# Kernel tuning notes

Hardware: AMD Instinct MI355X
Metric: run time of the kernel (lower is better)

## Reference

```python
import jax, jax.numpy as jnp
import numpy as np

K = 20
BN_EPS = 1e-5


def setup_inputs() -> dict:
    key = jax.random.key(0)
    ks = jax.random.split(key, 8)
    B, N, C = 4, 8192, 128
    x = jax.random.normal(ks[0], (B, C, N), dtype=jnp.float32)
    xyz = jax.random.normal(ks[1], (B, N, 3), dtype=jnp.float32)
    # Conv1d(C+3 -> C, kernel_size=1): weight [C, C+3], bias [C]
    w1 = jax.random.normal(ks[2], (C, C + 3), dtype=jnp.float32) * 0.05
    b1 = jax.random.normal(ks[3], (C,), dtype=jnp.float32) * 0.05
    gamma = jnp.ones((C,), dtype=jnp.float32)
    beta = jnp.zeros((C,), dtype=jnp.float32)
    # Conv1d(C -> C, kernel_size=1)
    w2 = jax.random.normal(ks[4], (C, C), dtype=jnp.float32) * 0.05
    b2 = jax.random.normal(ks[5], (C,), dtype=jnp.float32) * 0.05
    return {"x": x, "xyz": xyz, "w1": w1, "b1": b1, "gamma": gamma,
            "beta": beta, "w2": w2, "b2": b2}


def _compute_normals(xyz):
    # xyz: [B, N, 3]
    sq = jnp.sum(xyz * xyz, axis=-1)                      # [B, N]
    dist = (-2.0 * jnp.einsum('bnc,bmc->bnm', xyz, xyz)
            + sq[:, :, None] + sq[:, None, :])            # [B, N, N]
    _, idx = jax.lax.top_k(-dist, K)                      # smallest-k -> [B, N, k]
    neighbors = jax.vmap(lambda pts, ix: pts[ix])(xyz, idx)  # [B, N, k, 3]
    nb = neighbors - xyz[:, :, None, :]                   # centered
    cov = jnp.einsum('bnkc,bnkd->bncd', nb, nb)           # [B, N, 3, 3]
    _, eigvecs = jnp.linalg.eigh(cov)                     # ascending eigenvalues
    return eigvecs[..., :, 0]                             # normal = smallest-eig vector, [B, N, 3]


def reference(x, xyz, w1, b1, gamma, beta, w2, b2):
    normals = _compute_normals(xyz)                       # [B, N, 3]
    geo = jnp.concatenate([x, jnp.transpose(normals, (0, 2, 1))], axis=1)  # [B, C+3, N]
    h = jnp.einsum('oc,bcn->bon', w1, geo) + b1[None, :, None]
    # BatchNorm1d (training mode, biased variance over (B, N))
    mean = jnp.mean(h, axis=(0, 2), keepdims=True)
    var = jnp.mean((h - mean) ** 2, axis=(0, 2), keepdims=True)
    h = gamma[None, :, None] * (h - mean) * jax.lax.rsqrt(var + BN_EPS) + beta[None, :, None]
    h = jax.nn.relu(h)
    out = jnp.einsum('oc,bcn->bon', w2, h) + b2[None, :, None]
    return out
```

## Files before the change

kernel.cpp:

```cpp
#include <hip/hip_runtime.h>
#include <math.h>

#define N_PTS 8192
#define BATCH 4
#define CH 128
#define KNN 20
#define CAP 91
#define STQ 93
#define POOL 256


__device__ __forceinline__ float slapy2f(float x, float y) {
#pragma clang fp contract(off)
  float ax = fabsf(x), ay = fabsf(y);
  float w = fmaxf(ax, ay), z = fminf(ax, ay);
  if (z == 0.0f) return w;
  float t = z / w;
  return w * sqrtf(1.0f + t * t);
}

__device__ __forceinline__ void slartgf(float f, float g, float* cs, float* sn, float* r) {
#pragma clang fp contract(off)
  if (g == 0.0f) { *cs = 1.0f; *sn = 0.0f; *r = f; }
  else if (f == 0.0f) { *cs = 0.0f; *sn = copysignf(1.0f, g); *r = fabsf(g); }
  else {
    float f1 = fabsf(f);
    float d = sqrtf(f * f + g * g);
    *cs = f1 / d;
    *r = copysignf(d, f);
    *sn = g / (*r);
  }
}

__device__ void slaev2f(float a, float b, float c, float* rt1, float* rt2,
                        float* cs1, float* sn1) {
#pragma clang fp contract(off)
  float sm = a + c, df = a - c, adf = fabsf(df);
  float tb = b + b, ab = fabsf(tb);
  float acmx, acmn;
  if (fabsf(a) > fabsf(c)) { acmx = a; acmn = c; } else { acmx = c; acmn = a; }
  float rt;
  if (adf > ab)      { float q = ab / adf;  rt = adf * sqrtf(1.0f + q * q); }
  else if (adf < ab) { float q = adf / ab;  rt = ab * sqrtf(1.0f + q * q); }
  else               rt = ab * sqrtf(2.0f);
  int sgn1;
  if (sm < 0.0f)      { *rt1 = 0.5f * (sm - rt); sgn1 = -1; *rt2 = (acmx / *rt1) * acmn - (b / *rt1) * b; }
  else if (sm > 0.0f) { *rt1 = 0.5f * (sm + rt); sgn1 = 1;  *rt2 = (acmx / *rt1) * acmn - (b / *rt1) * b; }
  else                { *rt1 = 0.5f * rt; *rt2 = -0.5f * rt; sgn1 = 1; }
  float cs; int sgn2;
  if (df >= 0.0f) { cs = df + rt; sgn2 = 1; } else { cs = df - rt; sgn2 = -1; }
  float acs = fabsf(cs);
  if (acs > ab) {
    float ct = -tb / cs;
    *sn1 = 1.0f / sqrtf(1.0f + ct * ct);
    *cs1 = ct * (*sn1);
  } else {
    if (ab == 0.0f) { *cs1 = 1.0f; *sn1 = 0.0f; }
    else {
      float tn = -cs / tb;
      *cs1 = 1.0f / sqrtf(1.0f + tn * tn);
      *sn1 = tn * (*cs1);
    }
  }
  if (sgn1 == sgn2) { float tn = *cs1; *cs1 = -(*sn1); *sn1 = tn; }
}

__device__ void eigh3_smallest(float a00, float a10, float a20,
                               float a11, float a21, float a22, float evec[3]) {
#pragma clang fp contract(off)
  float d[3], e[2], tau = 0.0f, v2 = 0.0f;
  d[0] = a00;
  {
    float xnorm = sqrtf(a20 * a20);
    if (xnorm == 0.0f) {
      tau = 0.0f; v2 = 0.0f;
      e[0] = a10; d[1] = a11; e[1] = a21; d[2] = a22;
    } else {
      float alpha = a10;
      float beta = -copysignf(slapy2f(alpha, xnorm), alpha);
      tau = (beta - alpha) / beta;
      float invs = 1.0f / (alpha - beta);
      v2 = a20 * invs;
      e[0] = beta;
      float y0 = tau * a11;
      float y1 = tau * a21;
      y0 = y0 + tau * (a21 * v2);
      y1 = y1 + (tau * v2) * a22;
      float dot = y0 + y1 * v2;
      float al = (-0.5f * tau) * dot;
      float w0 = y0 + al;
      float w1 = y1 + al * v2;
      a11 = (a11 - w0) - w0;
      a21 = (a21 - v2 * w0) - w1;
      a22 = (a22 - v2 * w1) - w1 * v2;
      d[1] = a11; e[1] = a21; d[2] = a22;
    }
  }

  float z[3][3] = {{1.0f,0.0f,0.0f},{0.0f,1.0f,0.0f},{0.0f,0.0f,1.0f}};
  const float eps = 5.9604644775390625e-08f;
  const float eps2 = 3.5527136788005009e-15f;
  const float safmin = 1.1754943508222875e-38f;
  int nmaxit = 90, jtot = 0;
  int l1 = 0;
  int l, m, lend, lsv, lendsv;
  float p, g, r, c, s, f, b_, rt1, rt2, tst;
  float wc[2], wsn[2];

outer_loop:
  if (l1 > 2) goto sorting;
  if (l1 > 0) e[l1 - 1] = 0.0f;
  {
    int mm;
    for (mm = l1; mm <= 1; ++mm) {
      tst = fabsf(e[mm]);
      if (tst == 0.0f) break;
      if (tst <= (sqrtf(fabsf(d[mm])) * sqrtf(fabsf(d[mm + 1]))) * eps) { e[mm] = 0.0f; break; }
    }
    m = (mm > 1) ? 2 : mm;
  }
  l = l1; lsv = l; lend = m; lendsv = lend; l1 = m + 1;
  if (lend == l) goto outer_loop;
  {
    float an = 0.0f;
    for (int i2 = l; i2 <= lend; ++i2) an = fmaxf(an, fabsf(d[i2]));
    for (int i2 = l; i2 < lend; ++i2) an = fmaxf(an, fabsf(e[i2]));
    if (an == 0.0f) goto outer_loop;
  }
  if (fabsf(d[lend]) < fabsf(d[l])) { lend = lsv; l = lendsv; }

  if (lend > l) {
ql40:
    if (l != lend) {
      for (m = l; m <= lend - 1; ++m) {
        tst = e[m] * e[m];
        if (tst <= (eps2 * fabsf(d[m])) * fabsf(d[m + 1]) + safmin) goto ql60;
      }
    }
    m = lend;
ql60:
    if (m < lend) e[m] = 0.0f;
    p = d[l];
    if (m == l) goto ql80;
    if (m == l + 1) {
      slaev2f(d[l], e[l], d[l + 1], &rt1, &rt2, &c, &s);
      for (int i2 = 0; i2 < 3; ++i2) {
        float temp = z[i2][l + 1];
        z[i2][l + 1] = c * temp - s * z[i2][l];
        z[i2][l]     = s * temp + c * z[i2][l];
      }
      d[l] = rt1; d[l + 1] = rt2; e[l] = 0.0f;
      l += 2;
      if (l <= lend) goto ql40;
      goto done140;
    }
    if (jtot == nmaxit) goto done140;
    jtot++;
    g = (d[l + 1] - p) / (2.0f * e[l]);
    r = slapy2f(g, 1.0f);
    g = d[m] - p + e[l] / (g + copysignf(r, g));
    s = 1.0f; c = 1.0f; p = 0.0f;
    for (int i2 = m - 1; i2 >= l; --i2) {
      f = s * e[i2]; b_ = c * e[i2];
      slartgf(g, f, &c, &s, &r);
      if (i2 != m - 1) e[i2 + 1] = r;
      g = d[i2 + 1] - p;
      r = (d[i2] - g) * s + 2.0f * c * b_;
      p = s * r;
      d[i2 + 1] = g + p;
      g = c * r - b_;
      wc[i2] = c; wsn[i2] = -s;
    }
    for (int j = m - 1; j >= l; --j) {
      float ct = wc[j], st = wsn[j];
      for (int i2 = 0; i2 < 3; ++i2) {
        float temp = z[i2][j + 1];
        z[i2][j + 1] = ct * temp - st * z[i2][j];
        z[i2][j]     = st * temp + ct * z[i2][j];
      }
    }
    d[l] -= p;
    e[l] = g;
    goto ql40;
ql80:
    d[l] = p;
    l += 1;
    if (l <= lend) goto ql40;
    goto done140;
  } else {
qr90:
    if (l != lend) {
      for (m = l; m >= lend + 1; --m) {
        tst = e[m - 1] * e[m - 1];
        if (tst <= (eps2 * fabsf(d[m])) * fabsf(d[m - 1]) + safmin) goto qr110;
      }
    }
    m = lend;
qr110:
    if (m > lend) e[m - 1] = 0.0f;
    p = d[l];
    if (m == l) goto qr130;
    if (m == l - 1) {
      slaev2f(d[l - 1], e[l - 1], d[l], &rt1, &rt2, &c, &s);
      for (int i2 = 0; i2 < 3; ++i2) {
        float temp = z[i2][l];
        z[i2][l]     = c * temp - s * z[i2][l - 1];
        z[i2][l - 1] = s * temp + c * z[i2][l - 1];
      }
      d[l - 1] = rt1; d[l] = rt2; e[l - 1] = 0.0f;
      l -= 2;
      if (l >= lend) goto qr90;
      goto done140;
    }
    if (jtot == nmaxit) goto done140;
    jtot++;
    g = (d[l - 1] - p) / (2.0f * e[l - 1]);
    r = slapy2f(g, 1.0f);
    g = d[m] - p + e[l - 1] / (g + copysignf(r, g));
    s = 1.0f; c = 1.0f; p = 0.0f;
    for (int i2 = m; i2 <= l - 1; ++i2) {
      f = s * e[i2]; b_ = c * e[i2];
      slartgf(g, f, &c, &s, &r);
      if (i2 != m) e[i2 - 1] = r;
      g = d[i2] - p;
      r = (d[i2 + 1] - g) * s + 2.0f * c * b_;
      p = s * r;
      d[i2] = g + p;
      g = c * r - b_;
      wc[i2] = c; wsn[i2] = s;
    }
    for (int j = m; j <= l - 1; ++j) {
      float ct = wc[j], st = wsn[j];
      for (int i2 = 0; i2 < 3; ++i2) {
        float temp = z[i2][j + 1];
        z[i2][j + 1] = ct * temp - st * z[i2][j];
        z[i2][j]     = st * temp + ct * z[i2][j];
      }
    }
    d[l] -= p;
    e[l - 1] = g;
    goto qr90;
qr130:
    d[l] = p;
    l -= 1;
    if (l >= lend) goto qr90;
    goto done140;
  }
done140:
  if (jtot < nmaxit) goto outer_loop;
sorting:
  for (int ii = 1; ii <= 2; ++ii) {
    int i_ = ii - 1, k = i_;
    p = d[i_];
    for (int j = ii; j <= 2; ++j) if (d[j] < p) { k = j; p = d[j]; }
    if (k != i_) {
      d[k] = d[i_]; d[i_] = p;
      for (int i2 = 0; i2 < 3; ++i2) { float tz = z[i2][i_]; z[i2][i_] = z[i2][k]; z[i2][k] = tz; }
    }
  }
  {
    float z10 = z[1][0], z20 = z[2][0];
    float sum = z10 + v2 * z20;
    evec[0] = z[0][0];
    evec[1] = z10 - tau * sum;
    evec[2] = z20 - tau * sum * v2;
  }
}

__global__ __launch_bounds__(256) void prep_kernel(const float* __restrict__ xyz,
                                                   const float* __restrict__ w1,
                                                   const float* __restrict__ w2,
                                                   float4* __restrict__ xyz4,
                                                   float* __restrict__ w1t,
                                                   float* __restrict__ w2t,
                                                   float* __restrict__ stats) {
  int idx = blockIdx.x * 256 + threadIdx.x;
  if (idx < BATCH * N_PTS) {
    float x = xyz[idx * 3], y = xyz[idx * 3 + 1], zz = xyz[idx * 3 + 2];
    float sq = fmaf(zz, zz, fmaf(y, y, x * x));
    xyz4[idx] = make_float4(x, y, zz, -0.5f * sq);
  }
  if (idx < 132 * CH) {
    int cc = idx >> 7, o = idx & 127;
    w1t[idx] = (cc < 131) ? w1[o * 131 + cc] : 0.0f;
  }
  if (idx < CH * CH) {
    int cc = idx >> 7, o = idx & 127;
    w2t[idx] = w2[o * CH + cc];
  }
  if (idx < 256) stats[idx] = 0.0f;
}

__device__ __forceinline__ float qdist2(const float4 qv, const float4 cv) {
  float dot = fmaf(qv.x, cv.x, fmaf(qv.y, cv.y, qv.z * cv.z));
  return fmaf(-2.0f, dot, (-2.0f * qv.w) + (-2.0f * cv.w));
}

__device__ __forceinline__ unsigned int distbits(float dist) {
  unsigned int du = __float_as_uint(dist);
  return (du & 0x80000000u) ? ~du : (du | 0x80000000u);
}

__global__ __launch_bounds__(512, 8) void knn_select_kernel(const float4* __restrict__ xyz4,
                                                            unsigned short* __restrict__ nidx) {
  __shared__ unsigned long long pool[POOL];
  __shared__ unsigned int lst_d[64 * STQ];
  __shared__ unsigned short lst_i[64 * STQ];
  __shared__ float bnd[8 * 64];
  __shared__ unsigned int qcnt[64];
  __shared__ unsigned int qflag[64];
  __shared__ unsigned int qover[64];
  __shared__ unsigned int pool_cnt;

  const int t = threadIdx.x;
  const int w = t >> 6, l = t & 63;
  const int batch = blockIdx.x >> 7;
  const int q0 = (blockIdx.x & 127) << 6;
  const float4* __restrict__ xb = xyz4 + batch * N_PTS;
  const float4 qv = xb[q0 + l];
  const float qw = -2.0f * qv.w;

  if (t < 64) { qcnt[t] = 0; qflag[t] = 0; qover[t] = 0; }
  if (t == 0) pool_cnt = 0;
  __syncthreads();

  const int base = __builtin_amdgcn_readfirstlane(w * 1024);

  float c0 = -INFINITY, c1 = -INFINITY, c2 = -INFINITY;
#pragma unroll 8
  for (int i = 0; i < 1024; ++i) {
    float4 cv = xb[base + i];
    float k = fmaf(qv.x, cv.x, fmaf(qv.y, cv.y, fmaf(qv.z, cv.z, cv.w)));
    float t0 = fminf(c0, k); c0 = fmaxf(c0, k);
    float t1 = fminf(c1, t0); c1 = fmaxf(c1, t0);
    c2 = fmaxf(c2, t1);
  }
  bnd[w * 64 + l] = c2;
  __syncthreads();

  float kmin = bnd[l];
#pragma unroll
  for (int ww = 1; ww < 8; ++ww) kmin = fminf(kmin, bnd[ww * 64 + l]);
  float Tq = fmaf(-2.0f, kmin, qw);
  Tq = Tq + (fabsf(Tq) * 2e-5f + 1e-3f);
  const float thK = 0.5f * (qw - Tq) - 1e-3f;

#pragma unroll 4
  for (int i = 0; i < 1024; ++i) {
    float4 cv = xb[base + i];
    float k = fmaf(qv.x, cv.x, fmaf(qv.y, cv.y, fmaf(qv.z, cv.z, cv.w)));
    if (k >= thK) {
      float dot = fmaf(qv.x, cv.x, fmaf(qv.y, cv.y, qv.z * cv.z));
      float dist = fmaf(-2.0f, dot, qw + (-2.0f * cv.w));
      if (dist <= Tq) {
        unsigned int db = distbits(dist);
        unsigned int pos = atomicAdd(&qcnt[l], 1u);
        if (pos < CAP) {
          lst_d[l * STQ + pos] = db;
          lst_i[l * STQ + pos] = (unsigned short)(base + i);
        } else {
          unsigned long long key = ((unsigned long long)db << 32)
                                 | ((unsigned int)l << 16) | (unsigned int)(base + i);
          unsigned int pp = atomicAdd(&pool_cnt, 1u);
          if (pp < POOL) { pool[pp] = key; qflag[l] = 1u; }
          else qover[l] = 1u;
        }
      }
    }
  }
  __syncthreads();

  const int qg = t >> 3, sub = t & 7;
  unsigned int n = qcnt[qg]; if (n > CAP) n = CAP;
  const unsigned int pcnt = (qflag[qg] && !qover[qg]) ? min(pool_cnt, (unsigned int)POOL) : 0u;
  unsigned short* oq = nidx + ((size_t)(batch * N_PTS + q0 + qg)) * KNN;

  if (qover[qg]) {
    if (sub == 0) {
      unsigned long long best[KNN];
#pragma unroll
      for (int j = 0; j < KNN; ++j) best[j] = ~0ULL;
      const float4 qv2 = xb[q0 + qg];
      for (int m = 0; m < N_PTS; ++m) {
        float dist = qdist2(qv2, xb[m]);
        unsigned long long p = ((unsigned long long)distbits(dist) << 32) | (unsigned int)m;
        if (p < best[KNN - 1]) {
          int j = KNN - 1;
          while (j > 0 && best[j - 1] > p) { best[j] = best[j - 1]; --j; }
          best[j] = p;
        }
      }
      for (int j = 0; j < KNN; ++j) oq[j] = (unsigned short)(best[j] & 0xffffu);
    }
  } else {
    for (int r = 0; r < KNN; ++r) {
      unsigned long long best = ~0ULL; int bslot = 0;
      for (unsigned int s = sub; s < n; s += 8) {
        unsigned long long v = ((unsigned long long)lst_d[qg * STQ + s] << 16)
                             | (unsigned long long)lst_i[qg * STQ + s];
        if (v < best) { best = v; bslot = (int)s; }
      }
      for (unsigned int s = sub; s < pcnt; s += 8) {
        unsigned long long v = pool[s];
        if ((unsigned int)((v >> 16) & 0xffffu) == (unsigned int)qg) {
          unsigned long long pv = ((v >> 32) << 16) | (v & 0xffffULL);
          if (pv < best) { best = pv; bslot = 0x10000 | (int)s; }
        }
      }
#pragma unroll
      for (int mm = 1; mm < 8; mm <<= 1) {
        unsigned long long ob = __shfl_xor(best, mm, 64);
        int obs = __shfl_xor(bslot, mm, 64);
        if (ob < best) { best = ob; bslot = obs; }
      }
      int s = bslot & 0xffff;
      if ((s & 7) == sub) {
        if (bslot & 0x10000) pool[s] = ~0ULL;
        else lst_d[qg * STQ + s] = 0xFFFFFFFFu;
      }
      if (sub == 0) oq[r] = (unsigned short)(best & 0xffffu);
    }
  }
}

__global__ __launch_bounds__(256) void normals_kernel(const float4* __restrict__ xyz4,
                                                      const unsigned short* __restrict__ nidx,
                                                      float4* __restrict__ nrm4) {
  int gid = blockIdx.x * 256 + threadIdx.x;
  int batch = gid >> 13, q = gid & (N_PTS - 1);
  const float4* __restrict__ xb = xyz4 + batch * N_PTS;
  const float4 qv = xb[q];
  const unsigned short* iq = nidx + (size_t)gid * KNN;
  float c00, c01, c02, c11, c12, c22;
  {
#pragma clang fp contract(off)
    c00 = 0.f; c01 = 0.f; c02 = 0.f; c11 = 0.f; c12 = 0.f; c22 = 0.f;
    for (int j = 0; j < KNN; ++j) {
      float4 pv = xb[iq[j]];
      float dx = pv.x - qv.x, dy = pv.y - qv.y, dz = pv.z - qv.z;
      c00 = c00 + dx * dx; c01 = c01 + dx * dy; c02 = c02 + dx * dz;
      c11 = c11 + dy * dy; c12 = c12 + dy * dz; c22 = c22 + dz * dz;
    }
  }
  float ev[3];
  eigh3_smallest(c00, c01, c02, c11, c12, c22, ev);
  nrm4[gid] = make_float4(ev[0], ev[1], ev[2], 0.0f);
}

__global__ __launch_bounds__(256) void gemm1_stats_kernel(const float* __restrict__ x,
                                                          const float4* __restrict__ nrm4,
                                                          const float* __restrict__ w1t,
                                                          const float* __restrict__ b1,
                                                          float* __restrict__ sums,
                                                          float* __restrict__ sumsq) {
  __shared__ float lds[64 * 134];
  const int t = threadIdx.x;
  const int b = blockIdx.x >> 7;
  const int n0 = (blockIdx.x & 127) << 6;
  for (int idx = t; idx < CH * 64; idx += 256) {
    int cc = idx >> 6, nl = idx & 63;
    lds[nl * 134 + cc] = x[((size_t)(b * CH + cc)) * N_PTS + n0 + nl];
  }
  if (t < 64) {
    float4 nv = nrm4[b * N_PTS + n0 + t];
    lds[t * 134 + 128] = nv.x; lds[t * 134 + 129] = nv.y;
    lds[t * 134 + 130] = nv.z; lds[t * 134 + 131] = 0.0f;
  }
  __syncthreads();

  const int og = __builtin_amdgcn_readfirstlane(t >> 6);
  const int nl = t & 63;
  float acc[32];
#pragma unroll
  for (int k = 0; k < 32; ++k) acc[k] = b1[og * 32 + k];
  for (int c2 = 0; c2 < 66; ++c2) {
    float2 xv = *(const float2*)&lds[nl * 134 + 2 * c2];
    const float* wr0 = w1t + (2 * c2) * CH + og * 32;
    const float* wr1 = wr0 + CH;
#pragma unroll
    for (int k = 0; k < 32; ++k) acc[k] = fmaf(wr0[k], xv.x, acc[k]);
#pragma unroll
    for (int k = 0; k < 32; ++k) acc[k] = fmaf(wr1[k], xv.y, acc[k]);
  }
  __syncthreads();
#pragma unroll
  for (int k2 = 0; k2 < 16; ++k2)
    *(float2*)&lds[nl * 134 + og * 32 + 2 * k2] = make_float2(acc[2 * k2], acc[2 * k2 + 1]);
  __syncthreads();
  {
    int cc = t & 127, hf = t >> 7;
    float sm = 0.f, sq = 0.f;
    for (int rr = hf * 32; rr < hf * 32 + 32; ++rr) {
      float v = lds[rr * 134 + cc];
      sm += v; sq = fmaf(v, v, sq);
    }
    atomicAdd(&sums[cc], sm);
    atomicAdd(&sumsq[cc], sq);
  }
}

__global__ void bn_finalize_kernel(const float* __restrict__ sums, const float* __restrict__ sumsq,
                                   const float* __restrict__ gamma, const float* __restrict__ beta,
                                   float* __restrict__ scale, float* __restrict__ shift) {
  int c = threadIdx.x;
  if (c < CH) {
    const double cnt = (double)(BATCH * N_PTS);
    double mean = (double)sums[c] / cnt;
    double var = (double)sumsq[c] / cnt - mean * mean;
    double inv = 1.0 / sqrt(var + 1e-5);
    double sc = (double)gamma[c] * inv;
    scale[c] = (float)sc;
    shift[c] = (float)((double)beta[c] - mean * sc);
  }
}

__global__ __launch_bounds__(256) void fused_out_kernel(const float* __restrict__ x,
                                                        const float4* __restrict__ nrm4,
                                                        const float* __restrict__ w1t,
                                                        const float* __restrict__ b1,
                                                        const float* __restrict__ w2t,
                                                        const float* __restrict__ b2,
                                                        const float* __restrict__ scale,
                                                        const float* __restrict__ shift,
                                                        float* __restrict__ out) {
  __shared__ float lds[64 * 134];
  const int t = threadIdx.x;
  const int b = blockIdx.x >> 7;
  const int n0 = (blockIdx.x & 127) << 6;
  for (int idx = t; idx < CH * 64; idx += 256) {
    int cc = idx >> 6, nl = idx & 63;
    lds[nl * 134 + cc] = x[((size_t)(b * CH + cc)) * N_PTS + n0 + nl];
  }
  if (t < 64) {
    float4 nv = nrm4[b * N_PTS + n0 + t];
    lds[t * 134 + 128] = nv.x; lds[t * 134 + 129] = nv.y;
    lds[t * 134 + 130] = nv.z; lds[t * 134 + 131] = 0.0f;
  }
  __syncthreads();

  const int og = __builtin_amdgcn_readfirstlane(t >> 6);
  const int nl = t & 63;
  float acc[32];
#pragma unroll
  for (int k = 0; k < 32; ++k) acc[k] = b1[og * 32 + k];
  for (int c2 = 0; c2 < 66; ++c2) {
    float2 xv = *(const float2*)&lds[nl * 134 + 2 * c2];
    const float* wr0 = w1t + (2 * c2) * CH + og * 32;
    const float* wr1 = wr0 + CH;
#pragma unroll
    for (int k = 0; k < 32; ++k) acc[k] = fmaf(wr0[k], xv.x, acc[k]);
#pragma unroll
    for (int k = 0; k < 32; ++k) acc[k] = fmaf(wr1[k], xv.y, acc[k]);
  }
#pragma unroll
  for (int k = 0; k < 32; ++k) {
    float sc = scale[og * 32 + k], sh = shift[og * 32 + k];
    acc[k] = fmaxf(fmaf(acc[k], sc, sh), 0.0f);
  }
  __syncthreads();
#pragma unroll
  for (int k2 = 0; k2 < 16; ++k2)
    *(float2*)&lds[nl * 134 + og * 32 + 2 * k2] = make_float2(acc[2 * k2], acc[2 * k2 + 1]);
  __syncthreads();

  float acc2[32];
#pragma unroll
  for (int k = 0; k < 32; ++k) acc2[k] = b2[og * 32 + k];
  for (int c2 = 0; c2 < 64; ++c2) {
    float2 hv = *(const float2*)&lds[nl * 134 + 2 * c2];
    const float* wr0 = w2t + (2 * c2) * CH + og * 32;
    const float* wr1 = wr0 + CH;
#pragma unroll
    for (int k = 0; k < 32; ++k) acc2[k] = fmaf(wr0[k], hv.x, acc2[k]);
#pragma unroll
    for (int k = 0; k < 32; ++k) acc2[k] = fmaf(wr1[k], hv.y, acc2[k]);
  }
#pragma unroll
  for (int k = 0; k < 32; ++k) {
    int o = og * 32 + k;
    out[((size_t)(b * CH + o)) * N_PTS + n0 + nl] = acc2[k];
  }
}

extern "C" void kernel_launch(void* const* d_in, const int* in_sizes, int n_in,
                              void* d_out, int out_size, void* d_ws, size_t ws_size,
                              hipStream_t stream) {
  const float* x     = (const float*)d_in[0];
  const float* xyz   = (const float*)d_in[1];
  const float* w1    = (const float*)d_in[2];
  const float* b1    = (const float*)d_in[3];
  const float* gamma = (const float*)d_in[4];
  const float* beta  = (const float*)d_in[5];
  const float* w2    = (const float*)d_in[6];
  const float* b2    = (const float*)d_in[7];
  float* out = (float*)d_out;

  float* W = (float*)d_ws;
  float4* xyz4 = (float4*)W;
  float4* nrm4 = (float4*)(W + 131072);
  float* w1t   = W + 262144;
  float* w2t   = W + 279040;
  float* stats = W + 295424;
  float* scale = W + 295680;
  float* shift = W + 295808;
  unsigned short* nidx = (unsigned short*)(W + 295936);

  prep_kernel<<<128, 256, 0, stream>>>(xyz, w1, w2, xyz4, w1t, w2t, stats);
  knn_select_kernel<<<BATCH * N_PTS / 64, 512, 0, stream>>>(xyz4, nidx);
  normals_kernel<<<BATCH * N_PTS / 256, 256, 0, stream>>>(xyz4, nidx, nrm4);
  gemm1_stats_kernel<<<BATCH * N_PTS / 64, 256, 0, stream>>>(x, nrm4, w1t, b1, stats, stats + 128);
  bn_finalize_kernel<<<1, 128, 0, stream>>>(stats, stats + 128, gamma, beta, scale, shift);
  fused_out_kernel<<<BATCH * N_PTS / 64, 256, 0, stream>>>(x, nrm4, w1t, b1, w2t, b2, scale, shift, out);
}
```

Baseline: 396.3 us.

## Process two query groups per 1024-thread KNN block and shrink normals blocks

The KNN select kernel now handles 128 queries per block with 16 waves, each scanning 512 candidates. Each wave keeps a top-2 per query and merges wave pairs to get a third-smallest bound. Candidate loads are shared across the two query sets in the bound pass, and the bound buffer is aliased with the candidate lists in shared memory. The two query halves are filtered and selected one after the other, with 16 lanes per query in the selection step, and the list capacity is raised. The normals kernel switches to 64-thread blocks. This cuts repeated candidate reads and raises selection parallelism, at the cost of a looser threshold, more barriers and a larger block footprint.

```diff
diff --git a/kernel.cpp b/kernel.cpp
--- a/kernel.cpp
+++ b/kernel.cpp
@@ -5,9 +5,11 @@
 #define BATCH 4
 #define CH 128
 #define KNN 20
-#define CAP 91
-#define STQ 93
+#define CAP 112
+#define STQ 114
 #define POOL 256
+#define QPB 128
+#define NW 16
 
 
 __device__ __forceinline__ float slapy2f(float x, float y) {
@@ -301,58 +303,78 @@
   return (du & 0x80000000u) ? ~du : (du | 0x80000000u);
 }
 
-__global__ __launch_bounds__(512, 8) void knn_select_kernel(const float4* __restrict__ xyz4,
-                                                            unsigned short* __restrict__ nidx) {
+__global__ __launch_bounds__(1024) void knn_select_kernel(const float4* __restrict__ xyz4,
+                                                          unsigned short* __restrict__ nidx) {
+  __shared__ alignas(16) unsigned char smem[64 * STQ * 6];
   __shared__ unsigned long long pool[POOL];
-  __shared__ unsigned int lst_d[64 * STQ];
-  __shared__ unsigned short lst_i[64 * STQ];
-  __shared__ float bnd[8 * 64];
   __shared__ unsigned int qcnt[64];
   __shared__ unsigned int qflag[64];
   __shared__ unsigned int qover[64];
   __shared__ unsigned int pool_cnt;
 
+  float2* bnd2 = reinterpret_cast<float2*>(smem);
+  unsigned int* lst_d = reinterpret_cast<unsigned int*>(smem);
+  unsigned short* lst_i = reinterpret_cast<unsigned short*>(smem + 64 * STQ * 4);
+
   const int t = threadIdx.x;
   const int w = t >> 6, l = t & 63;
-  const int batch = blockIdx.x >> 7;
-  const int q0 = (blockIdx.x & 127) << 6;
+  const int batch = blockIdx.x >> 6;
+  const int q0 = (blockIdx.x & 63) << 7;
   const float4* __restrict__ xb = xyz4 + batch * N_PTS;
-  const float4 qv = xb[q0 + l];
-  const float qw = -2.0f * qv.w;
-
+  const float4 qvA = xb[q0 + l];
+  const float4 qvB = xb[q0 + 64 + l];
+  const float qwA = -2.0f * qvA.w;
+  const float qwB = -2.0f * qvB.w;
+
+  const int base = __builtin_amdgcn_readfirstlane(w << 9);
+
+  float a0 = -INFINITY, a1 = -INFINITY;
+  float c0 = -INFINITY, c1 = -INFINITY;
+#pragma unroll 8
+  for (int i = 0; i < 512; ++i) {
+    float4 cv = xb[base + i];
+    float kA = fmaf(qvA.x, cv.x, fmaf(qvA.y, cv.y, fmaf(qvA.z, cv.z, cv.w)));
+    float kB = fmaf(qvB.x, cv.x, fmaf(qvB.y, cv.y, fmaf(qvB.z, cv.z, cv.w)));
+    float tA = fminf(a0, kA); a0 = fmaxf(a0, kA); a1 = fmaxf(a1, tA);
+    float tB = fminf(c0, kB); c0 = fmaxf(c0, kB); c1 = fmaxf(c1, tB);
+  }
+  bnd2[w * 128 + l]      = make_float2(a0, a1);
+  bnd2[w * 128 + 64 + l] = make_float2(c0, c1);
+  __syncthreads();
+
+  float TqA, thKA, TqB, thKB;
+  {
+    float kminA = INFINITY, kminB = INFINITY;
+#pragma unroll
+    for (int g = 0; g < 8; ++g) {
+      float2 pa = bnd2[(2 * g) * 128 + l];
+      float2 pb = bnd2[(2 * g + 1) * 128 + l];
+      float v3 = fmaxf(fminf(pa.y, pb.x), fminf(pa.x, pb.y));
+      kminA = fminf(kminA, v3);
+      float2 qa = bnd2[(2 * g) * 128 + 64 + l];
+      float2 qb = bnd2[(2 * g + 1) * 128 + 64 + l];
+      float u3 = fmaxf(fminf(qa.y, qb.x), fminf(qa.x, qb.y));
+      kminB = fminf(kminB, u3);
+    }
+    TqA = fmaf(-2.0f, kminA, qwA);
+    TqA = TqA + (fabsf(TqA) * 2e-5f + 1e-3f);
+    thKA = 0.5f * (qwA - TqA) - 1e-3f;
+    TqB = fmaf(-2.0f, kminB, qwB);
+    TqB = TqB + (fabsf(TqB) * 2e-5f + 1e-3f);
+    thKB = 0.5f * (qwB - TqB) - 1e-3f;
+  }
   if (t < 64) { qcnt[t] = 0; qflag[t] = 0; qover[t] = 0; }
   if (t == 0) pool_cnt = 0;
   __syncthreads();
 
-  const int base = __builtin_amdgcn_readfirstlane(w * 1024);
-
-  float c0 = -INFINITY, c1 = -INFINITY, c2 = -INFINITY;
-#pragma unroll 8
-  for (int i = 0; i < 1024; ++i) {
+#pragma unroll 4
+  for (int i = 0; i < 512; ++i) {
     float4 cv = xb[base + i];
-    float k = fmaf(qv.x, cv.x, fmaf(qv.y, cv.y, fmaf(qv.z, cv.z, cv.w)));
-    float t0 = fminf(c0, k); c0 = fmaxf(c0, k);
-    float t1 = fminf(c1, t0); c1 = fmaxf(c1, t0);
-    c2 = fmaxf(c2, t1);
-  }
-  bnd[w * 64 + l] = c2;
-  __syncthreads();
-
-  float kmin = bnd[l];
-#pragma unroll
-  for (int ww = 1; ww < 8; ++ww) kmin = fminf(kmin, bnd[ww * 64 + l]);
-  float Tq = fmaf(-2.0f, kmin, qw);
-  Tq = Tq + (fabsf(Tq) * 2e-5f + 1e-3f);
-  const float thK = 0.5f * (qw - Tq) - 1e-3f;
-
-#pragma unroll 4
-  for (int i = 0; i < 1024; ++i) {
-    float4 cv = xb[base + i];
-    float k = fmaf(qv.x, cv.x, fmaf(qv.y, cv.y, fmaf(qv.z, cv.z, cv.w)));
-    if (k >= thK) {
-      float dot = fmaf(qv.x, cv.x, fmaf(qv.y, cv.y, qv.z * cv.z));
-      float dist = fmaf(-2.0f, dot, qw + (-2.0f * cv.w));
-      if (dist <= Tq) {
+    float k = fmaf(qvA.x, cv.x, fmaf(qvA.y, cv.y, fmaf(qvA.z, cv.z, cv.w)));
+    if (k >= thKA) {
+      float dot = fmaf(qvA.x, cv.x, fmaf(qvA.y, cv.y, qvA.z * cv.z));
+      float dist = fmaf(-2.0f, dot, qwA + (-2.0f * cv.w));
+      if (dist <= TqA) {
         unsigned int db = distbits(dist);
         unsigned int pos = atomicAdd(&qcnt[l], 1u);
         if (pos < CAP) {
@@ -370,63 +392,149 @@
   }
   __syncthreads();
 
-  const int qg = t >> 3, sub = t & 7;
-  unsigned int n = qcnt[qg]; if (n > CAP) n = CAP;
-  const unsigned int pcnt = (qflag[qg] && !qover[qg]) ? min(pool_cnt, (unsigned int)POOL) : 0u;
-  unsigned short* oq = nidx + ((size_t)(batch * N_PTS + q0 + qg)) * KNN;
-
-  if (qover[qg]) {
-    if (sub == 0) {
-      unsigned long long best[KNN];
-#pragma unroll
-      for (int j = 0; j < KNN; ++j) best[j] = ~0ULL;
-      const float4 qv2 = xb[q0 + qg];
-      for (int m = 0; m < N_PTS; ++m) {
-        float dist = qdist2(qv2, xb[m]);
-        unsigned long long p = ((unsigned long long)distbits(dist) << 32) | (unsigned int)m;
-        if (p < best[KNN - 1]) {
-          int j = KNN - 1;
-          while (j > 0 && best[j - 1] > p) { best[j] = best[j - 1]; --j; }
-          best[j] = p;
-        }
-      }
-      for (int j = 0; j < KNN; ++j) oq[j] = (unsigned short)(best[j] & 0xffffu);
-    }
-  } else {
-    for (int r = 0; r < KNN; ++r) {
-      unsigned long long best = ~0ULL; int bslot = 0;
-      for (unsigned int s = sub; s < n; s += 8) {
-        unsigned long long v = ((unsigned long long)lst_d[qg * STQ + s] << 16)
-                             | (unsigned long long)lst_i[qg * STQ + s];
-        if (v < best) { best = v; bslot = (int)s; }
-      }
-      for (unsigned int s = sub; s < pcnt; s += 8) {
-        unsigned long long v = pool[s];
-        if ((unsigned int)((v >> 16) & 0xffffu) == (unsigned int)qg) {
-          unsigned long long pv = ((v >> 32) << 16) | (v & 0xffffULL);
-          if (pv < best) { best = pv; bslot = 0x10000 | (int)s; }
-        }
-      }
-#pragma unroll
-      for (int mm = 1; mm < 8; mm <<= 1) {
-        unsigned long long ob = __shfl_xor(best, mm, 64);
-        int obs = __shfl_xor(bslot, mm, 64);
-        if (ob < best) { best = ob; bslot = obs; }
-      }
-      int s = bslot & 0xffff;
-      if ((s & 7) == sub) {
-        if (bslot & 0x10000) pool[s] = ~0ULL;
-        else lst_d[qg * STQ + s] = 0xFFFFFFFFu;
-      }
-      if (sub == 0) oq[r] = (unsigned short)(best & 0xffffu);
-    }
-  }
-}
-
-__global__ __launch_bounds__(256) void normals_kernel(const float4* __restrict__ xyz4,
-                                                      const unsigned short* __restrict__ nidx,
-                                                      float4* __restrict__ nrm4) {
-  int gid = blockIdx.x * 256 + threadIdx.x;
+  {
+    const int qg = t >> 4, sub = t & 15;
+    unsigned int n = qcnt[qg]; if (n > CAP) n = CAP;
+    const unsigned int pcnt = (qflag[qg] && !qover[qg]) ? min(pool_cnt, (unsigned int)POOL) : 0u;
+    unsigned short* oq = nidx + ((size_t)(batch * N_PTS + q0 + qg)) * KNN;
+
+    if (qover[qg]) {
+      if (sub == 0) {
+        unsigned long long best[KNN];
+#pragma unroll
+        for (int j = 0; j < KNN; ++j) best[j] = ~0ULL;
+        const float4 qv2 = xb[q0 + qg];
+        for (int m = 0; m < N_PTS; ++m) {
+          float dist = qdist2(qv2, xb[m]);
+          unsigned long long p = ((unsigned long long)distbits(dist) << 32) | (unsigned int)m;
+          if (p < best[KNN - 1]) {
+            int j = KNN - 1;
+            while (j > 0 && best[j - 1] > p) { best[j] = best[j - 1]; --j; }
+            best[j] = p;
+          }
+        }
+        for (int j = 0; j < KNN; ++j) oq[j] = (unsigned short)(best[j] & 0xffffu);
+      }
+    } else {
+      for (int r = 0; r < KNN; ++r) {
+        unsigned long long best = ~0ULL; int bslot = 0;
+        for (unsigned int s = sub; s < n; s += 16) {
+          unsigned long long v = ((unsigned long long)lst_d[qg * STQ + s] << 16)
+                               | (unsigned long long)lst_i[qg * STQ + s];
+          if (v < best) { best = v; bslot = (int)s; }
+        }
+        for (unsigned int s = sub; s < pcnt; s += 16) {
+          unsigned long long v = pool[s];
+          if ((unsigned int)((v >> 16) & 0xffffu) == (unsigned int)qg) {
+            unsigned long long pv = ((v >> 32) << 16) | (v & 0xffffULL);
+            if (pv < best) { best = pv; bslot = 0x10000 | (int)s; }
+          }
+        }
+#pragma unroll
+        for (int mm = 1; mm < 16; mm <<= 1) {
+          unsigned long long ob = __shfl_xor(best, mm, 64);
+          int obs = __shfl_xor(bslot, mm, 64);
+          if (ob < best) { best = ob; bslot = obs; }
+        }
+        int s = bslot & 0xffff;
+        if ((s & 15) == sub) {
+          if (bslot & 0x10000) pool[s] = ~0ULL;
+          else lst_d[qg * STQ + s] = 0xFFFFFFFFu;
+        }
+        if (sub == 0) oq[r] = (unsigned short)(best & 0xffffu);
+      }
+    }
+  }
+  __syncthreads();
+
+  if (t < 64) { qcnt[t] = 0; qflag[t] = 0; qover[t] = 0; }
+  if (t == 0) pool_cnt = 0;
+  __syncthreads();
+
+#pragma unroll 4
+  for (int i = 0; i < 512; ++i) {
+    float4 cv = xb[base + i];
+    float k = fmaf(qvB.x, cv.x, fmaf(qvB.y, cv.y, fmaf(qvB.z, cv.z, cv.w)));
+    if (k >= thKB) {
+      float dot = fmaf(qvB.x, cv.x, fmaf(qvB.y, cv.y, qvB.z * cv.z));
+      float dist = fmaf(-2.0f, dot, qwB + (-2.0f * cv.w));
+      if (dist <= TqB) {
+        unsigned int db = distbits(dist);
+        unsigned int pos = atomicAdd(&qcnt[l], 1u);
+        if (pos < CAP) {
+          lst_d[l * STQ + pos] = db;
+          lst_i[l * STQ + pos] = (unsigned short)(base + i);
+        } else {
+          unsigned long long key = ((unsigned long long)db << 32)
+                                 | ((unsigned int)l << 16) | (unsigned int)(base + i);
+          unsigned int pp = atomicAdd(&pool_cnt, 1u);
+          if (pp < POOL) { pool[pp] = key; qflag[l] = 1u; }
+          else qover[l] = 1u;
+        }
+      }
+    }
+  }
+  __syncthreads();
+
+  {
+    const int qg = t >> 4, sub = t & 15;
+    unsigned int n = qcnt[qg]; if (n > CAP) n = CAP;
+    const unsigned int pcnt = (qflag[qg] && !qover[qg]) ? min(pool_cnt, (unsigned int)POOL) : 0u;
+    unsigned short* oq = nidx + ((size_t)(batch * N_PTS + q0 + 64 + qg)) * KNN;
+
+    if (qover[qg]) {
+      if (sub == 0) {
+        unsigned long long best[KNN];
+#pragma unroll
+        for (int j = 0; j < KNN; ++j) best[j] = ~0ULL;
+        const float4 qv2 = xb[q0 + 64 + qg];
+        for (int m = 0; m < N_PTS; ++m) {
+          float dist = qdist2(qv2, xb[m]);
+          unsigned long long p = ((unsigned long long)distbits(dist) << 32) | (unsigned int)m;
+          if (p < best[KNN - 1]) {
+            int j = KNN - 1;
+            while (j > 0 && best[j - 1] > p) { best[j] = best[j - 1]; --j; }
+            best[j] = p;
+          }
+        }
+        for (int j = 0; j < KNN; ++j) oq[j] = (unsigned short)(best[j] & 0xffffu);
+      }
+    } else {
+      for (int r = 0; r < KNN; ++r) {
+        unsigned long long best = ~0ULL; int bslot = 0;
+        for (unsigned int s = sub; s < n; s += 16) {
+          unsigned long long v = ((unsigned long long)lst_d[qg * STQ + s] << 16)
+                               | (unsigned long long)lst_i[qg * STQ + s];
+          if (v < best) { best = v; bslot = (int)s; }
+        }
+        for (unsigned int s = sub; s < pcnt; s += 16) {
+          unsigned long long v = pool[s];
+          if ((unsigned int)((v >> 16) & 0xffffu) == (unsigned int)qg) {
+            unsigned long long pv = ((v >> 32) << 16) | (v & 0xffffULL);
+            if (pv < best) { best = pv; bslot = 0x10000 | (int)s; }
+          }
+        }
+#pragma unroll
+        for (int mm = 1; mm < 16; mm <<= 1) {
+          unsigned long long ob = __shfl_xor(best, mm, 64);
+          int obs = __shfl_xor(bslot, mm, 64);
+          if (ob < best) { best = ob; bslot = obs; }
+        }
+        int s = bslot & 0xffff;
+        if ((s & 15) == sub) {
+          if (bslot & 0x10000) pool[s] = ~0ULL;
+          else lst_d[qg * STQ + s] = 0xFFFFFFFFu;
+        }
+        if (sub == 0) oq[r] = (unsigned short)(best & 0xffffu);
+      }
+    }
+  }
+}
+
+__global__ __launch_bounds__(64) void normals_kernel(const float4* __restrict__ xyz4,
+                                                     const unsigned short* __restrict__ nidx,
+                                                     float4* __restrict__ nrm4) {
+  int gid = blockIdx.x * 64 + threadIdx.x;
   int batch = gid >> 13, q = gid & (N_PTS - 1);
   const float4* __restrict__ xb = xyz4 + batch * N_PTS;
   const float4 qv = xb[q];
@@ -606,8 +714,8 @@
   unsigned short* nidx = (unsigned short*)(W + 295936);
 
   prep_kernel<<<128, 256, 0, stream>>>(xyz, w1, w2, xyz4, w1t, w2t, stats);
-  knn_select_kernel<<<BATCH * N_PTS / 64, 512, 0, stream>>>(xyz4, nidx);
-  normals_kernel<<<BATCH * N_PTS / 256, 256, 0, stream>>>(xyz4, nidx, nrm4);
+  knn_select_kernel<<<BATCH * N_PTS / QPB, 1024, 0, stream>>>(xyz4, nidx);
+  normals_kernel<<<BATCH * N_PTS / 64, 64, 0, stream>>>(xyz4, nidx, nrm4);
   gemm1_stats_kernel<<<BATCH * N_PTS / 64, 256, 0, stream>>>(x, nrm4, w1t, b1, stats, stats + 128);
   bn_finalize_kernel<<<1, 128, 0, stream>>>(stats, stats + 128, gamma, beta, scale, shift);
   fused_out_kernel<<<BATCH * N_PTS / 64, 256, 0, stream>>>(x, nrm4, w1t, b1, w2t, b2, scale, shift, out);
```

New measurement: 418.6 us. +5.6%, slower.

## Split KNN candidate scan across 16 waves with pairwise top-3 threshold merge

Applied to the files above, without the earlier changes.

The KNN select kernel now launches 1024 threads, so each wave scans 512 candidates instead of 1024, with a small register prefetch buffer in both passes. Each wave keeps its top three keys, and adjacent waves' lists are merged to get a tighter per-query pruning bound. Per-query list capacity grows and the final top-20 extraction uses 16 lanes per query instead of 8. The normals kernel moves to 64-thread blocks. The larger shared-memory footprint and 1024-thread blocks may limit how many blocks fit per CU, and the prefetch reads a few entries past each batch's slice.

```diff
diff --git a/kernel.cpp b/kernel.cpp
--- a/kernel.cpp
+++ b/kernel.cpp
@@ -5,8 +5,8 @@
 #define BATCH 4
 #define CH 128
 #define KNN 20
-#define CAP 91
-#define STQ 93
+#define CAP 112
+#define STQ 114
 #define POOL 256
 
 
@@ -301,12 +301,12 @@
   return (du & 0x80000000u) ? ~du : (du | 0x80000000u);
 }
 
-__global__ __launch_bounds__(512, 8) void knn_select_kernel(const float4* __restrict__ xyz4,
-                                                            unsigned short* __restrict__ nidx) {
-  __shared__ unsigned long long pool[POOL];
+__global__ __launch_bounds__(1024, 8) void knn_select_kernel(const float4* __restrict__ xyz4,
+                                                             unsigned short* __restrict__ nidx) {
   __shared__ unsigned int lst_d[64 * STQ];
   __shared__ unsigned short lst_i[64 * STQ];
-  __shared__ float bnd[8 * 64];
+  __shared__ float bnd[16 * 64 * 3];
+  __shared__ unsigned long long pool[POOL];
   __shared__ unsigned int qcnt[64];
   __shared__ unsigned int qflag[64];
   __shared__ unsigned int qover[64];
@@ -322,55 +322,80 @@
 
   if (t < 64) { qcnt[t] = 0; qflag[t] = 0; qover[t] = 0; }
   if (t == 0) pool_cnt = 0;
-  __syncthreads();
-
-  const int base = __builtin_amdgcn_readfirstlane(w * 1024);
-
-  float c0 = -INFINITY, c1 = -INFINITY, c2 = -INFINITY;
-#pragma unroll 8
-  for (int i = 0; i < 1024; ++i) {
-    float4 cv = xb[base + i];
-    float k = fmaf(qv.x, cv.x, fmaf(qv.y, cv.y, fmaf(qv.z, cv.z, cv.w)));
-    float t0 = fminf(c0, k); c0 = fmaxf(c0, k);
-    float t1 = fminf(c1, t0); c1 = fmaxf(c1, t0);
-    c2 = fmaxf(c2, t1);
-  }
-  bnd[w * 64 + l] = c2;
-  __syncthreads();
-
-  float kmin = bnd[l];
-#pragma unroll
-  for (int ww = 1; ww < 8; ++ww) kmin = fminf(kmin, bnd[ww * 64 + l]);
+
+  const int base = __builtin_amdgcn_readfirstlane(w * 512);
+
+  float a0 = -INFINITY, a1 = -INFINITY, a2 = -INFINITY;
+  {
+    float4 buf[4];
+#pragma unroll
+    for (int j = 0; j < 4; ++j) buf[j] = xb[base + j];
+    for (int i = 0; i < 512; i += 4) {
+#pragma unroll
+      for (int j = 0; j < 4; ++j) {
+        float4 cv = buf[j];
+        buf[j] = xb[base + i + 4 + j];
+        float k = fmaf(qv.x, cv.x, fmaf(qv.y, cv.y, fmaf(qv.z, cv.z, cv.w)));
+        float t0 = fminf(a0, k); a0 = fmaxf(a0, k);
+        float t1 = fminf(a1, t0); a1 = fmaxf(a1, t0);
+        a2 = fmaxf(a2, t1);
+      }
+    }
+  }
+  {
+    int bi = (w * 64 + l) * 3;
+    bnd[bi] = a0; bnd[bi + 1] = a1; bnd[bi + 2] = a2;
+  }
+  __syncthreads();
+
+  float kmin = INFINITY;
+#pragma unroll
+  for (int g = 0; g < 8; ++g) {
+    int ai = ((2 * g) * 64 + l) * 3;
+    int bi = ((2 * g + 1) * 64 + l) * 3;
+    float pa0 = bnd[ai], pa1 = bnd[ai + 1], pa2 = bnd[ai + 2];
+    float pb0 = bnd[bi], pb1 = bnd[bi + 1], pb2 = bnd[bi + 2];
+    float third = fmaxf(fmaxf(pa2, pb2), fmaxf(fminf(pa1, pb0), fminf(pa0, pb1)));
+    kmin = fminf(kmin, third);
+  }
   float Tq = fmaf(-2.0f, kmin, qw);
   Tq = Tq + (fabsf(Tq) * 2e-5f + 1e-3f);
   const float thK = 0.5f * (qw - Tq) - 1e-3f;
 
-#pragma unroll 4
-  for (int i = 0; i < 1024; ++i) {
-    float4 cv = xb[base + i];
-    float k = fmaf(qv.x, cv.x, fmaf(qv.y, cv.y, fmaf(qv.z, cv.z, cv.w)));
-    if (k >= thK) {
-      float dot = fmaf(qv.x, cv.x, fmaf(qv.y, cv.y, qv.z * cv.z));
-      float dist = fmaf(-2.0f, dot, qw + (-2.0f * cv.w));
-      if (dist <= Tq) {
-        unsigned int db = distbits(dist);
-        unsigned int pos = atomicAdd(&qcnt[l], 1u);
-        if (pos < CAP) {
-          lst_d[l * STQ + pos] = db;
-          lst_i[l * STQ + pos] = (unsigned short)(base + i);
-        } else {
-          unsigned long long key = ((unsigned long long)db << 32)
-                                 | ((unsigned int)l << 16) | (unsigned int)(base + i);
-          unsigned int pp = atomicAdd(&pool_cnt, 1u);
-          if (pp < POOL) { pool[pp] = key; qflag[l] = 1u; }
-          else qover[l] = 1u;
+  {
+    float4 buf[4];
+#pragma unroll
+    for (int j = 0; j < 4; ++j) buf[j] = xb[base + j];
+    for (int i = 0; i < 512; i += 4) {
+#pragma unroll
+      for (int j = 0; j < 4; ++j) {
+        float4 cv = buf[j];
+        buf[j] = xb[base + i + 4 + j];
+        float k = fmaf(qv.x, cv.x, fmaf(qv.y, cv.y, fmaf(qv.z, cv.z, cv.w)));
+        if (k >= thK) {
+          float dot = fmaf(qv.x, cv.x, fmaf(qv.y, cv.y, qv.z * cv.z));
+          float dist = fmaf(-2.0f, dot, qw + (-2.0f * cv.w));
+          if (dist <= Tq) {
+            unsigned int db = distbits(dist);
+            unsigned int pos = atomicAdd(&qcnt[l], 1u);
+            if (pos < CAP) {
+              lst_d[l * STQ + pos] = db;
+              lst_i[l * STQ + pos] = (unsigned short)(base + i + j);
+            } else {
+              unsigned long long key = ((unsigned long long)db << 32)
+                                     | ((unsigned int)l << 16) | (unsigned int)(base + i + j);
+              unsigned int pp = atomicAdd(&pool_cnt, 1u);
+              if (pp < POOL) { pool[pp] = key; qflag[l] = 1u; }
+              else qover[l] = 1u;
+            }
+          }
         }
       }
     }
   }
   __syncthreads();
 
-  const int qg = t >> 3, sub = t & 7;
+  const int qg = t >> 4, sub = t & 15;
   unsigned int n = qcnt[qg]; if (n > CAP) n = CAP;
   const unsigned int pcnt = (qflag[qg] && !qover[qg]) ? min(pool_cnt, (unsigned int)POOL) : 0u;
   unsigned short* oq = nidx + ((size_t)(batch * N_PTS + q0 + qg)) * KNN;
@@ -395,12 +420,12 @@
   } else {
     for (int r = 0; r < KNN; ++r) {
       unsigned long long best = ~0ULL; int bslot = 0;
-      for (unsigned int s = sub; s < n; s += 8) {
+      for (unsigned int s = sub; s < n; s += 16) {
         unsigned long long v = ((unsigned long long)lst_d[qg * STQ + s] << 16)
                              | (unsigned long long)lst_i[qg * STQ + s];
         if (v < best) { best = v; bslot = (int)s; }
       }
-      for (unsigned int s = sub; s < pcnt; s += 8) {
+      for (unsigned int s = sub; s < pcnt; s += 16) {
         unsigned long long v = pool[s];
         if ((unsigned int)((v >> 16) & 0xffffu) == (unsigned int)qg) {
           unsigned long long pv = ((v >> 32) << 16) | (v & 0xffffULL);
@@ -408,13 +433,13 @@
         }
       }
 #pragma unroll
-      for (int mm = 1; mm < 8; mm <<= 1) {
+      for (int mm = 1; mm < 16; mm <<= 1) {
         unsigned long long ob = __shfl_xor(best, mm, 64);
         int obs = __shfl_xor(bslot, mm, 64);
         if (ob < best) { best = ob; bslot = obs; }
       }
       int s = bslot & 0xffff;
-      if ((s & 7) == sub) {
+      if ((s & 15) == sub) {
         if (bslot & 0x10000) pool[s] = ~0ULL;
         else lst_d[qg * STQ + s] = 0xFFFFFFFFu;
       }
@@ -423,10 +448,10 @@
   }
 }
 
-__global__ __launch_bounds__(256) void normals_kernel(const float4* __restrict__ xyz4,
-                                                      const unsigned short* __restrict__ nidx,
-                                                      float4* __restrict__ nrm4) {
-  int gid = blockIdx.x * 256 + threadIdx.x;
+__global__ __launch_bounds__(64) void normals_kernel(const float4* __restrict__ xyz4,
+                                                     const unsigned short* __restrict__ nidx,
+                                                     float4* __restrict__ nrm4) {
+  int gid = blockIdx.x * 64 + threadIdx.x;
   int batch = gid >> 13, q = gid & (N_PTS - 1);
   const float4* __restrict__ xb = xyz4 + batch * N_PTS;
   const float4 qv = xb[q];
@@ -606,8 +631,8 @@
   unsigned short* nidx = (unsigned short*)(W + 295936);
 
   prep_kernel<<<128, 256, 0, stream>>>(xyz, w1, w2, xyz4, w1t, w2t, stats);
-  knn_select_kernel<<<BATCH * N_PTS / 64, 512, 0, stream>>>(xyz4, nidx);
-  normals_kernel<<<BATCH * N_PTS / 256, 256, 0, stream>>>(xyz4, nidx, nrm4);
+  knn_select_kernel<<<BATCH * N_PTS / 64, 1024, 0, stream>>>(xyz4, nidx);
+  normals_kernel<<<BATCH * N_PTS / 64, 64, 0, stream>>>(xyz4, nidx, nrm4);
   gemm1_stats_kernel<<<BATCH * N_PTS / 64, 256, 0, stream>>>(x, nrm4, w1t, b1, stats, stats + 128);
   bn_finalize_kernel<<<1, 128, 0, stream>>>(stats, stats + 128, gamma, beta, scale, shift);
   fused_out_kernel<<<BATCH * N_PTS / 64, 256, 0, stream>>>(x, nrm4, w1t, b1, w2t, b2, scale, shift, out);
```

New measurement: 372.5 us. -6.0%, faster.
